# Kernel tuning notes

Hardware: AMD Instinct MI355X
Metric: run time of the kernel (lower is better)

## Reference

```python
import jax, jax.numpy as jnp
import numpy as np
from jax import lax

TEMPERATURE = 1.0
STRIDE = 1
PADDING = 1


def setup_inputs() -> dict:
    key = jax.random.key(0)
    ks = jax.random.split(key, 5)
    B, Cin, H, W = 32, 256, 56, 56
    Cout, K, kk = 256, 4, 3
    hidden = Cin // 4
    x = jax.random.normal(ks[0], (B, Cin, H, W), dtype=jnp.float32)
    weight_bank = jax.random.normal(ks[1], (K, Cout, Cin, kk, kk), dtype=jnp.float32) * 0.02
    fc1_w = jax.random.normal(ks[2], (hidden, Cin), dtype=jnp.float32) * (1.0 / np.sqrt(Cin))
    fc1_b = jnp.zeros((hidden,), dtype=jnp.float32)
    fc2_w = jax.random.normal(ks[3], (K, hidden), dtype=jnp.float32) * (1.0 / np.sqrt(hidden))
    fc2_b = jnp.zeros((K,), dtype=jnp.float32)
    return {"x": x, "weight_bank": weight_bank, "fc1_w": fc1_w,
            "fc1_b": fc1_b, "fc2_w": fc2_w, "fc2_b": fc2_b}


def reference(x, weight_bank, fc1_w, fc1_b, fc2_w, fc2_b):
    B, Cin, H, W = x.shape
    K, Cout = weight_bank.shape[0], weight_bank.shape[1]
    kk = weight_bank.shape[3]
    # Router: global average pool -> MLP -> softmax over K banks
    v = jnp.mean(x, axis=(2, 3))                      # [B, Cin]
    h = jax.nn.relu(v @ fc1_w.T + fc1_b)              # [B, hidden]
    logits = h @ fc2_w.T + fc2_b                      # [B, K]
    a = jax.nn.softmax(logits / TEMPERATURE, axis=1)  # [B, K]
    # Per-sample dynamic weight: mix the K banks
    Wdyn = jnp.einsum('bk,kocij->bocij', a, weight_bank)  # [B, Cout, Cin, k, k]
    # Batched per-sample conv via grouped convolution (groups=B)
    x2 = x.reshape(1, B * Cin, H, W)
    W2 = Wdyn.reshape(B * Cout, Cin, kk, kk)
    y = lax.conv_general_dilated(
        x2, W2,
        window_strides=(STRIDE, STRIDE),
        padding=((PADDING, PADDING), (PADDING, PADDING)),
        dimension_numbers=('NCHW', 'OIHW', 'NCHW'),
        feature_group_count=B,
    )
    Ho, Wo = y.shape[2], y.shape[3]
    return y.reshape(B, Cout, Ho, Wo)
```

## Files before the change

### kernel.cpp

```cpp
#include <hip/hip_runtime.h>
#include <stdint.h>

typedef unsigned short u16;
typedef unsigned int   u32;

#define B_SZ  32
#define CIN   256
#define NPIX  3136
#define COUT  256
#define HID   64
#define NBANK 4
#define BANK_SZ 589824
#define WF_N  18874368

#define XROWS 64
#define XSP_N 33554432ull

typedef _Float16 f16x8 __attribute__((ext_vector_type(8)));
typedef short bf16x8 __attribute__((ext_vector_type(8)));
typedef float f32x4  __attribute__((ext_vector_type(4)));

struct __align__(16) U4 { u32 x, y, z, w; };
struct __align__(16) F4 { float x, y, z, w; };

__device__ __forceinline__ float bf2f(u16 u) {
    union { u32 i; float f; } v; v.i = ((u32)u) << 16; return v.f;
}
__device__ __forceinline__ u16 f2bf(float f) {
    union { float f; u32 i; } v; v.f = f;
    u32 u = v.i;
    return (u16)((u + 0x7FFFu + ((u >> 16) & 1u)) >> 16);
}
__device__ __forceinline__ u16 f2h(float f) {
    union { _Float16 h; u16 u; } v; v.h = (_Float16)f;
    return v.u;
}

__device__ __forceinline__ void gload_lds16(const u16* g, u16* l) {
    __builtin_amdgcn_global_load_lds(
        (const __attribute__((address_space(1))) void*)g,
        (__attribute__((address_space(3))) void*)l, 16, 0, 0);
}

__global__ __launch_bounds__(64) void k_mean(const float* __restrict__ x,
                                             float* __restrict__ vout) {
    int bc = blockIdx.x;
    const F4* p = (const F4*)(x + (size_t)bc * NPIX);
    float s = 0.f;
    for (int o = threadIdx.x; o < 784; o += 64) {
        F4 u = p[o];
        s += u.x + u.y + u.z + u.w;
    }
    #pragma unroll
    for (int off = 32; off > 0; off >>= 1) s += __shfl_down(s, off, 64);
    if (threadIdx.x == 0) vout[bc] = s * (1.0f / 3136.0f);
}

__global__ __launch_bounds__(64) void k_router(const float* __restrict__ v,
        const float* __restrict__ fc1w, const float* __restrict__ fc1b,
        const float* __restrict__ fc2w, const float* __restrict__ fc2b,
        float* __restrict__ aout) {
    int b = blockIdx.x, j = threadIdx.x;
    __shared__ float hl[HID];
    __shared__ float lg[NBANK];
    const float* vb = v + b * CIN;
    float acc = fc1b[j];
    const F4* wrow = (const F4*)(fc1w + j * CIN);
    for (int o = 0; o < 64; ++o) {
        F4 u = wrow[o];
        acc += vb[o * 4 + 0] * u.x + vb[o * 4 + 1] * u.y
             + vb[o * 4 + 2] * u.z + vb[o * 4 + 3] * u.w;
    }
    hl[j] = acc > 0.f ? acc : 0.f;
    __syncthreads();
    if (j < NBANK) {
        float l = fc2b[j];
        for (int t = 0; t < HID; ++t) l += hl[t] * fc2w[j * HID + t];
        lg[j] = l;
    }
    __syncthreads();
    if (j == 0) {
        float m = lg[0];
        for (int k = 1; k < NBANK; ++k) m = fmaxf(m, lg[k]);
        float e[NBANK], se = 0.f;
        for (int k = 0; k < NBANK; ++k) { e[k] = expf(lg[k] - m); se += e[k]; }
        for (int k = 0; k < NBANK; ++k) aout[b * NBANK + k] = e[k] / se;
    }
}

__global__ __launch_bounds__(256) void k_split(const float* __restrict__ x,
                                               u16* __restrict__ xsp) {
    const int blk = blockIdx.x;
    const int row = blk & 63;
    const int bc  = blk >> 6;
    const int b   = bc >> 3, cis = bc & 7;
    const int t   = threadIdx.x;
    const size_t obase = (size_t)blk * 2048;
    const int hin = row - 1;
    if (hin < 0 || hin >= 56) {
        U4 z; z.x = 0; z.y = 0; z.z = 0; z.w = 0;
        *(U4*)(xsp + obase + (size_t)t * 8) = z;
        return;
    }
    __shared__ float ls[32 * 57];
    const float* xb = x + ((size_t)b * CIN + cis * 32) * NPIX + hin * 56;
    for (int idx = t; idx < 448; idx += 256) {
        int ci = idx / 14, o = idx - ci * 14;
        F4 u = *(const F4*)(xb + (size_t)ci * NPIX + o * 4);
        float* d = &ls[ci * 57 + o * 4];
        d[0] = u.x; d[1] = u.y; d[2] = u.z; d[3] = u.w;
    }
    __syncthreads();
    const int ci2 = (t & 15) * 2;
    const int cg  = t >> 4;
    const int ciq = ci2 >> 3;
    const int cil = ci2 & 7;
    #pragma unroll
    for (int k = 0; k < 4; ++k) {
        int col = cg + k * 16;
        int win = col - 1;
        float v0 = 0.f, v1 = 0.f;
        if (win >= 0 && win < 56) {
            v0 = ls[ci2 * 57 + win];
            v1 = ls[(ci2 + 1) * 57 + win];
        }
        size_t pos = obase + (size_t)(ciq * 64 + col) * 8 + cil;
        *(u32*)(xsp + pos) = (u32)f2h(v0) | ((u32)f2h(v1) << 16);
    }
}

#define PM_PAD 145
__global__ __launch_bounds__(256) void k_premix(const float* __restrict__ bank,
        const float* __restrict__ aws, u16* __restrict__ wf) {
    int cof   = blockIdx.x >> 4;
    int cis16 = blockIdx.x & 15;
    int bgrp  = blockIdx.y;
    __shared__ float lw[64 * PM_PAD];
    for (int idx = threadIdx.x; idx < 64 * 144; idx += 256) {
        int s = idx / 144;
        int e = idx - s * 144;
        int k = s >> 4, co_l = s & 15;
        lw[s * PM_PAD + e] =
            bank[(size_t)(k * COUT + cof * 16 + co_l) * (CIN * 9) + cis16 * 144 + e];
    }
    __syncthreads();
    const int cis   = cis16 >> 1;
    const int qbase = (cis16 & 1) * 2;
    for (int b8 = 0; b8 < 8; ++b8) {
        const int b = bgrp * 8 + b8;
        float a0 = aws[b * 4 + 0], a1 = aws[b * 4 + 1];
        float a2 = aws[b * 4 + 2], a3 = aws[b * 4 + 3];
        for (int o = threadIdx.x; o < 288; o += 256) {
            int t  = o >> 5;
            int hlane = o & 31;
            int lane  = qbase * 16 + hlane;
            int m = lane & 15, q = lane >> 4;
            int q_loc = q - qbase;
            u16 ph[8];
            #pragma unroll
            for (int jj = 0; jj < 8; ++jj) {
                int ee = (q_loc * 8 + jj) * 9 + t;
                float w = a0 * lw[(0 * 16 + m) * PM_PAD + ee]
                        + a1 * lw[(1 * 16 + m) * PM_PAD + ee]
                        + a2 * lw[(2 * 16 + m) * PM_PAD + ee]
                        + a3 * lw[(3 * 16 + m) * PM_PAD + ee];
                ph[jj] = f2h(w);
            }
            size_t off = ((((size_t)b * 16 + cof) * 9 + t) * 8 + cis) * 512
                       + (size_t)lane * 8;
            U4 uh;
            uh.x = (u32)ph[0] | ((u32)ph[1] << 16);
            uh.y = (u32)ph[2] | ((u32)ph[3] << 16);
            uh.z = (u32)ph[4] | ((u32)ph[5] << 16);
            uh.w = (u32)ph[6] | ((u32)ph[7] << 16);
            *(U4*)(wf + off) = uh;
        }
    }
}

__global__ __launch_bounds__(256, 2) void k_conv2(
        const u16* __restrict__ wf,
        const u16* __restrict__ xsp,
        float* __restrict__ out) {
    __shared__ u16 xbuf[2][16384];

    const int flat = blockIdx.x;
    const int g    = flat & 7;
    const int idx  = flat >> 3;
    const int b    = g * 4 + (idx / 26);
    const int r    = idx % 26;
    const int coblk = r / 13;
    const int pt    = r % 13;

    const int tid  = threadIdx.x;
    const int wave = tid >> 6;
    const int lane = tid & 63;
    const int wm = wave >> 1, wn = wave & 1;

    const int pix0 = pt * 256;
    const int h0   = pix0 / 56;

    const size_t rowbase = (((size_t)b * 8) * 64 + h0) * 2048;

    int bb[8], pl[8];
    #pragma unroll
    for (int nf = 0; nf < 8; ++nf) {
        int p = pix0 + wn * 128 + nf * 16 + (lane & 15);
        pl[nf] = p;
        int pc = p < NPIX ? p : NPIX - 1;
        int hp = pc / 56, wp = pc - (pc / 56) * 56;
        bb[nf] = ((hp - h0) * 256 + (lane >> 4) * 64 + wp) * 16;
    }

    const u16* wbase = wf
        + ((size_t)b * 16 + coblk * 8 + wm * 4) * (9 * 8 * 512)
        + (size_t)lane * 8;

    f32x4 acc[4][8];
    #pragma unroll
    for (int i = 0; i < 4; ++i)
        #pragma unroll
        for (int j = 0; j < 8; ++j) { f32x4 z = {0.f, 0.f, 0.f, 0.f}; acc[i][j] = z; }

    {
        const u16* sb = xsp + rowbase;
        #pragma unroll
        for (int c = wave; c < 32; c += 4)
            gload_lds16(sb + c * 512 + lane * 8, &xbuf[0][c * 512 + lane * 8]);
    }

    for (int cis = 0; cis < 8; ++cis) {
        asm volatile("s_waitcnt vmcnt(0) lgkmcnt(0)" ::: "memory");
        __builtin_amdgcn_s_barrier();
        __builtin_amdgcn_sched_barrier(0);
        if (cis < 7) {
            const u16* sb = xsp + rowbase + (size_t)(cis + 1) * 131072;
            u16* db = &xbuf[(cis + 1) & 1][0];
            #pragma unroll
            for (int c = wave; c < 32; c += 4)
                gload_lds16(sb + c * 512 + lane * 8, db + c * 512 + lane * 8);
        }
        __builtin_amdgcn_sched_barrier(0);

        const char* xb = (const char*)&xbuf[cis & 1][0];
        f16x8 w[4][4];
        #pragma unroll
        for (int mf = 0; mf < 4; ++mf) {
            w[0][mf] = *(const f16x8*)(wbase + (size_t)((mf * 9 + 0) * 8 + cis) * 512);
            w[1][mf] = *(const f16x8*)(wbase + (size_t)((mf * 9 + 1) * 8 + cis) * 512);
            w[2][mf] = *(const f16x8*)(wbase + (size_t)((mf * 9 + 2) * 8 + cis) * 512);
        }
        #pragma unroll
        for (int t = 0; t < 9; ++t) {
            if (t < 6) {
                #pragma unroll
                for (int mf = 0; mf < 4; ++mf)
                    w[(t + 3) & 3][mf] =
                        *(const f16x8*)(wbase + (size_t)((mf * 9 + t + 3) * 8 + cis) * 512);
            }
            const int ty = t / 3, tx = t - ty * 3;
            const int toff = ty * 4096 + tx * 16;
            __builtin_amdgcn_s_setprio(1);
            #pragma unroll
            for (int nf = 0; nf < 8; ++nf) {
                f16x8 bx = *(const f16x8*)(xb + bb[nf] + toff);
                #pragma unroll
                for (int mf = 0; mf < 4; ++mf) {
                    acc[mf][nf] = __builtin_amdgcn_mfma_f32_16x16x32_f16(
                        w[t & 3][mf], bx, acc[mf][nf], 0, 0, 0);
                }
            }
            __builtin_amdgcn_s_setprio(0);
        }
    }

    float* ob = out + (size_t)b * COUT * NPIX;
    #pragma unroll
    for (int mf = 0; mf < 4; ++mf) {
        int cobase = coblk * 128 + wm * 64 + mf * 16 + (lane >> 4) * 4;
        #pragma unroll
        for (int nf = 0; nf < 8; ++nf) {
            int p = pl[nf];
            if (p < NPIX) {
                #pragma unroll
                for (int r = 0; r < 4; ++r)
                    ob[(size_t)(cobase + r) * NPIX + p] = acc[mf][nf][r];
            }
        }
    }
}

__global__ __launch_bounds__(256, 2) void k_conv_fb(const float* __restrict__ x,
        const float* __restrict__ bank,
        const float* __restrict__ aws,
        float* __restrict__ out) {
    const int pt    = blockIdx.x;
    const int coblk = blockIdx.y;
    const int b     = blockIdx.z;

    const int tid  = threadIdx.x;
    const int wave = tid >> 6;
    const int lane = tid & 63;
    const int wm = wave >> 1, wn = wave & 1;

    __shared__ u16 xs[2][6 * 58 * 32];

    const int pix0 = pt * 128;
    const int h0   = pix0 / 56;
    const int rlo  = h0 - 1;

    const float* xb = x + (size_t)b * CIN * NPIX;

    int bbase[4], pl[4];
    #pragma unroll
    for (int nf = 0; nf < 4; ++nf) {
        int p = pix0 + wn * 64 + nf * 16 + (lane & 15);
        pl[nf] = p;
        int pc = p < NPIX ? p : NPIX - 1;
        int hp = pc / 56, wp = pc - (pc / 56) * 56;
        bbase[nf] = ((hp - h0) * 58 + wp) * 64 + (lane >> 4) * 16;
    }

    float a0 = aws[b * 4 + 0], a1 = aws[b * 4 + 1];
    float a2 = aws[b * 4 + 2], a3 = aws[b * 4 + 3];

    f32x4 acc[4][4];
    #pragma unroll
    for (int i = 0; i < 4; ++i)
        #pragma unroll
        for (int j = 0; j < 4; ++j) { f32x4 z = {0.f, 0.f, 0.f, 0.f}; acc[i][j] = z; }

    for (int cis = 0; cis < 8; ++cis) {
        const int ci0 = cis * 32;
        __syncthreads();
        for (int idx = tid; idx < 1392; idx += 256) {
            int oct = idx / 348;
            int rc  = idx - oct * 348;
            int row = rc / 58, col = rc - row * 58;
            int hin = rlo + row, win = col - 1;
            U4 uh; uh.x = 0; uh.y = 0; uh.z = 0; uh.w = 0;
            U4 ul = uh;
            if (hin >= 0 && hin < 56 && win >= 0 && win < 56) {
                const float* gp = xb + (size_t)(ci0 + oct * 8) * NPIX + hin * 56 + win;
                u16 eh[8], el[8];
                #pragma unroll
                for (int i = 0; i < 8; ++i) {
                    float v = gp[(size_t)i * NPIX];
                    u16 h = f2bf(v);
                    eh[i] = h;
                    el[i] = f2bf(v - bf2f(h));
                }
                uh.x = (u32)eh[0] | ((u32)eh[1] << 16);
                uh.y = (u32)eh[2] | ((u32)eh[3] << 16);
                uh.z = (u32)eh[4] | ((u32)eh[5] << 16);
                uh.w = (u32)eh[6] | ((u32)eh[7] << 16);
                ul.x = (u32)el[0] | ((u32)el[1] << 16);
                ul.y = (u32)el[2] | ((u32)el[3] << 16);
                ul.z = (u32)el[4] | ((u32)el[5] << 16);
                ul.w = (u32)el[6] | ((u32)el[7] << 16);
            }
            *(U4*)(&xs[0][rc * 32 + oct * 8]) = uh;
            *(U4*)(&xs[1][rc * 32 + oct * 8]) = ul;
        }
        __syncthreads();

        #pragma unroll
        for (int t = 0; t < 9; ++t) {
            const int ty = t / 3, tx = t - (t / 3) * 3;
            bf16x8 ah[4], al[4];
            #pragma unroll
            for (int mf = 0; mf < 4; ++mf) {
                int co = coblk * 128 + wm * 64 + mf * 16 + (lane & 15);
                int q = lane >> 4;
                u16 ph[8], plo[8];
                #pragma unroll
                for (int jj = 0; jj < 8; ++jj) {
                    int ci = ci0 + q * 8 + jj;
                    size_t base = ((size_t)co * CIN + ci) * 9 + t;
                    float w = a0 * bank[base]
                            + a1 * bank[base + BANK_SZ]
                            + a2 * bank[base + 2 * BANK_SZ]
                            + a3 * bank[base + 3 * BANK_SZ];
                    u16 h = f2bf(w);
                    ph[jj]  = h;
                    plo[jj] = f2bf(w - bf2f(h));
                }
                union { U4 u; bf16x8 v; } pu;
                pu.u.x = (u32)ph[0] | ((u32)ph[1] << 16);
                pu.u.y = (u32)ph[2] | ((u32)ph[3] << 16);
                pu.u.z = (u32)ph[4] | ((u32)ph[5] << 16);
                pu.u.w = (u32)ph[6] | ((u32)ph[7] << 16);
                ah[mf] = pu.v;
                pu.u.x = (u32)plo[0] | ((u32)plo[1] << 16);
                pu.u.y = (u32)plo[2] | ((u32)plo[3] << 16);
                pu.u.z = (u32)plo[4] | ((u32)plo[5] << 16);
                pu.u.w = (u32)plo[6] | ((u32)plo[7] << 16);
                al[mf] = pu.v;
            }
            const int toff = (ty * 58 + tx) * 64;
            #pragma unroll
            for (int nf = 0; nf < 4; ++nf) {
                bf16x8 bh = *(const bf16x8*)((const char*)&xs[0][0] + bbase[nf] + toff);
                bf16x8 bl = *(const bf16x8*)((const char*)&xs[1][0] + bbase[nf] + toff);
                #pragma unroll
                for (int mf = 0; mf < 4; ++mf) {
                    acc[mf][nf] = __builtin_amdgcn_mfma_f32_16x16x32_bf16(
                        ah[mf], bh, acc[mf][nf], 0, 0, 0);
                    acc[mf][nf] = __builtin_amdgcn_mfma_f32_16x16x32_bf16(
                        ah[mf], bl, acc[mf][nf], 0, 0, 0);
                    acc[mf][nf] = __builtin_amdgcn_mfma_f32_16x16x32_bf16(
                        al[mf], bh, acc[mf][nf], 0, 0, 0);
                }
            }
        }
    }

    float* ob = out + (size_t)b * COUT * NPIX;
    #pragma unroll
    for (int mf = 0; mf < 4; ++mf) {
        int cobase = coblk * 128 + wm * 64 + mf * 16 + (lane >> 4) * 4;
        #pragma unroll
        for (int nf = 0; nf < 4; ++nf) {
            int p = pl[nf];
            if (p < NPIX) {
                #pragma unroll
                for (int r = 0; r < 4; ++r)
                    ob[(size_t)(cobase + r) * NPIX + p] = acc[mf][nf][r];
            }
        }
    }
}

extern "C" void kernel_launch(void* const* d_in, const int* in_sizes, int n_in,
                              void* d_out, int out_size, void* d_ws, size_t ws_size,
                              hipStream_t stream) {
    const float* x    = (const float*)d_in[0];
    const float* bank = (const float*)d_in[1];
    const float* fc1w = (const float*)d_in[2];
    const float* fc1b = (const float*)d_in[3];
    const float* fc2w = (const float*)d_in[4];
    const float* fc2b = (const float*)d_in[5];
    float* out = (float*)d_out;

    float* a_ws = (float*)d_ws;
    float* v_ws = (float*)d_ws + 128;
    u16*   wf   = (u16*)((char*)d_ws + 65536);
    u16*   xsp  = (u16*)((char*)d_ws + 65536 + (size_t)WF_N * sizeof(u16));

    const size_t need = (size_t)65536 + (size_t)WF_N * sizeof(u16)
                      + (size_t)XSP_N * sizeof(u16);

    k_mean<<<dim3(B_SZ * CIN), dim3(64), 0, stream>>>(x, v_ws);
    k_router<<<dim3(B_SZ), dim3(64), 0, stream>>>(v_ws, fc1w, fc1b, fc2w, fc2b, a_ws);

    if (ws_size >= need) {
        k_premix<<<dim3(256, 4), dim3(256), 0, stream>>>(bank, a_ws, wf);
        k_split<<<dim3(B_SZ * 8 * XROWS), dim3(256), 0, stream>>>(x, xsp);
        k_conv2<<<dim3(832), dim3(256), 0, stream>>>(wf, xsp, out);
    } else {
        k_conv_fb<<<dim3(25, 2, B_SZ), dim3(256), 0, stream>>>(x, bank, a_ws, out);
    }
}
```

Measured before the change: 360.7 us.

## Fuse mean pooling into split kernel and router into premix

The global average pool is now computed inside k_split from the rows already staged in shared memory, using atomicAdd into a zeroed buffer. The router MLP and softmax are recomputed per block inside k_premix. This removes a separate full read of x and two kernel launches, replacing them with one memset. The cost is atomic contention, a floating-point summation order that varies between runs, and the fc1 matvec being repeated in each of the 1024 premix blocks.

Result: slower. 395.2 us (+9.6%).

```diff
diff --git a/kernel.cpp b/kernel.cpp
--- a/kernel.cpp
+++ b/kernel.cpp
@@ -89,7 +89,8 @@
 }
 
 __global__ __launch_bounds__(256) void k_split(const float* __restrict__ x,
-                                               u16* __restrict__ xsp) {
+                                               u16* __restrict__ xsp,
+                                               float* __restrict__ vmean) {
     const int blk = blockIdx.x;
     const int row = blk & 63;
     const int bc  = blk >> 6;
@@ -111,6 +112,16 @@
         d[0] = u.x; d[1] = u.y; d[2] = u.z; d[3] = u.w;
     }
     __syncthreads();
+    {
+        int ci = t >> 3, part = t & 7;
+        const float* r = &ls[ci * 57 + part * 7];
+        float s = r[0] + r[1] + r[2] + r[3] + r[4] + r[5] + r[6];
+        s += __shfl_down(s, 4, 64);
+        s += __shfl_down(s, 2, 64);
+        s += __shfl_down(s, 1, 64);
+        if (part == 0)
+            atomicAdd(&vmean[b * CIN + cis * 32 + ci], s * (1.0f / 3136.0f));
+    }
     const int ci2 = (t & 15) * 2;
     const int cg  = t >> 4;
     const int ciq = ci2 >> 3;
@@ -131,11 +142,16 @@
 
 #define PM_PAD 145
 __global__ __launch_bounds__(256) void k_premix(const float* __restrict__ bank,
-        const float* __restrict__ aws, u16* __restrict__ wf) {
+        const float* __restrict__ vmean,
+        const float* __restrict__ fc1w, const float* __restrict__ fc1b,
+        const float* __restrict__ fc2w, const float* __restrict__ fc2b,
+        u16* __restrict__ wf) {
     int cof   = blockIdx.x >> 4;
     int cis16 = blockIdx.x & 15;
     int bgrp  = blockIdx.y;
     __shared__ float lw[64 * PM_PAD];
+    __shared__ float hlq[8][HID];
+    __shared__ float avals[8][NBANK];
     for (int idx = threadIdx.x; idx < 64 * 144; idx += 256) {
         int s = idx / 144;
         int e = idx - s * 144;
@@ -143,13 +159,43 @@
         lw[s * PM_PAD + e] =
             bank[(size_t)(k * COUT + cof * 16 + co_l) * (CIN * 9) + cis16 * 144 + e];
     }
+    {
+        const int wv = threadIdx.x >> 6, ln = threadIdx.x & 63;
+        #pragma unroll
+        for (int s2 = 0; s2 < 2; ++s2) {
+            const int b8 = wv * 2 + s2;
+            const float* vb = vmean + (bgrp * 8 + b8) * CIN;
+            float acc = fc1b[ln];
+            const F4* wrow = (const F4*)(fc1w + ln * CIN);
+            for (int o = 0; o < 64; ++o) {
+                F4 u = wrow[o];
+                acc += vb[o * 4 + 0] * u.x + vb[o * 4 + 1] * u.y
+                     + vb[o * 4 + 2] * u.z + vb[o * 4 + 3] * u.w;
+            }
+            hlq[b8][ln] = acc > 0.f ? acc : 0.f;
+        }
+    }
+    __syncthreads();
+    if (threadIdx.x < 32) {
+        const int b8 = threadIdx.x >> 2, k = threadIdx.x & 3;
+        float l = fc2b[k];
+        for (int t = 0; t < HID; ++t) l += hlq[b8][t] * fc2w[k * HID + t];
+        float m = l;
+        m = fmaxf(m, __shfl_xor(m, 1, 64));
+        m = fmaxf(m, __shfl_xor(m, 2, 64));
+        float e = expf(l - m);
+        float se = e;
+        se += __shfl_xor(se, 1, 64);
+        se += __shfl_xor(se, 2, 64);
+        avals[b8][k] = e / se;
+    }
     __syncthreads();
     const int cis   = cis16 >> 1;
     const int qbase = (cis16 & 1) * 2;
     for (int b8 = 0; b8 < 8; ++b8) {
         const int b = bgrp * 8 + b8;
-        float a0 = aws[b * 4 + 0], a1 = aws[b * 4 + 1];
-        float a2 = aws[b * 4 + 2], a3 = aws[b * 4 + 3];
+        float a0 = avals[b8][0], a1 = avals[b8][1];
+        float a2 = avals[b8][2], a3 = avals[b8][3];
         for (int o = threadIdx.x; o < 288; o += 256) {
             int t  = o >> 5;
             int hlane = o & 31;
@@ -450,14 +496,15 @@
     const size_t need = (size_t)65536 + (size_t)WF_N * sizeof(u16)
                       + (size_t)XSP_N * sizeof(u16);
 
-    k_mean<<<dim3(B_SZ * CIN), dim3(64), 0, stream>>>(x, v_ws);
-    k_router<<<dim3(B_SZ), dim3(64), 0, stream>>>(v_ws, fc1w, fc1b, fc2w, fc2b, a_ws);
-
     if (ws_size >= need) {
-        k_premix<<<dim3(256, 4), dim3(256), 0, stream>>>(bank, a_ws, wf);
-        k_split<<<dim3(B_SZ * 8 * XROWS), dim3(256), 0, stream>>>(x, xsp);
+        hipMemsetAsync(v_ws, 0, (size_t)B_SZ * CIN * sizeof(float), stream);
+        k_split<<<dim3(B_SZ * 8 * XROWS), dim3(256), 0, stream>>>(x, xsp, v_ws);
+        k_premix<<<dim3(256, 4), dim3(256), 0, stream>>>(bank, v_ws,
+                                                         fc1w, fc1b, fc2w, fc2b, wf);
         k_conv2<<<dim3(832), dim3(256), 0, stream>>>(wf, xsp, out);
     } else {
+        k_mean<<<dim3(B_SZ * CIN), dim3(64), 0, stream>>>(x, v_ws);
+        k_router<<<dim3(B_SZ), dim3(64), 0, stream>>>(v_ws, fc1w, fc1b, fc2w, fc2b, a_ws);
         k_conv_fb<<<dim3(25, 2, B_SZ), dim3(256), 0, stream>>>(x, bank, a_ws, out);
     }
 }
```
